# Performance work log

Hardware: AMD Instinct MI355X
Metric: run time of the kernel (lower is better)

Reference implementation:

```python
import jax, jax.numpy as jnp
import numpy as np

EMBED, IN_DIM, HID, LAYERS, NVIEW = 1024, 256, 256, 3, 6


def _lstm_layer(x_seq, Wih, Whh, bih, bhh):
    # x_seq: [BM, N, D]; torch LSTM gate order i,f,g,o
    BM = x_seq.shape[0]
    h0 = jnp.zeros((BM, HID), x_seq.dtype)
    c0 = jnp.zeros((BM, HID), x_seq.dtype)

    def step(carry, x_t):
        h, c = carry
        gates = x_t @ Wih.T + bih + h @ Whh.T + bhh  # [BM, 4H]
        i, f, g, o = jnp.split(gates, 4, axis=-1)
        c = jax.nn.sigmoid(f) * c + jax.nn.sigmoid(i) * jnp.tanh(g)
        h = jax.nn.sigmoid(o) * jnp.tanh(c)
        return (h, c), h

    _, ys = jax.lax.scan(step, (h0, c0), jnp.swapaxes(x_seq, 0, 1))
    return jnp.swapaxes(ys, 0, 1)  # [BM, N, H]


def setup_inputs() -> dict:
    key = jax.random.key(0)
    ks = jax.random.split(key, 16)
    B, M = 32, 256
    s = lambda fan: 1.0 / np.sqrt(fan)
    inp = {
        "b_x_swin": jax.random.normal(ks[0], (B, M, NVIEW, EMBED), jnp.float32),
        "b_x_conv": jax.random.normal(ks[1], (B, M, NVIEW, EMBED), jnp.float32),
        "Wc": jax.random.uniform(ks[2], (EMBED, EMBED), jnp.float32, -s(EMBED), s(EMBED)),
        "bc": jax.random.uniform(ks[3], (EMBED,), jnp.float32, -s(EMBED), s(EMBED)),
        "Win": jax.random.uniform(ks[4], (IN_DIM, EMBED), jnp.float32, -s(EMBED), s(EMBED)),
        "b_in": jax.random.uniform(ks[5], (IN_DIM,), jnp.float32, -s(EMBED), s(EMBED)),
        "Wih": jax.random.uniform(ks[6], (LAYERS, 4 * HID, IN_DIM), jnp.float32, -s(HID), s(HID)),
        "Whh": jax.random.uniform(ks[7], (LAYERS, 4 * HID, HID), jnp.float32, -s(HID), s(HID)),
        "bih": jax.random.uniform(ks[8], (LAYERS, 4 * HID), jnp.float32, -s(HID), s(HID)),
        "bhh": jax.random.uniform(ks[9], (LAYERS, 4 * HID), jnp.float32, -s(HID), s(HID)),
        "Wv": jax.random.uniform(ks[10], (1, HID), jnp.float32, -s(HID), s(HID)),
        "bv": jax.random.uniform(ks[11], (1,), jnp.float32, -s(HID), s(HID)),
        "Ws": jax.random.uniform(ks[12], (1, NVIEW), jnp.float32, -s(NVIEW), s(NVIEW)),
        "bs": jax.random.uniform(ks[13], (1,), jnp.float32, -s(NVIEW), s(NVIEW)),
    }
    return inp


def reference(b_x_swin, b_x_conv, Wc, bc, Win, b_in, Wih, Whh, bih, bhh, Wv, bv, Ws, bs):
    B, M, N, C = b_x_swin.shape
    # fc_conv + exact GELU + residual (vectorized over all samples; same math as per-sample loop)
    x = b_x_swin + jax.nn.gelu(b_x_conv @ Wc.T + bc, approximate=False)
    x = x @ Win.T + b_in                         # [B, M, N, IN_DIM]
    x = x.reshape(B * M, N, IN_DIM)              # LSTM batch = B*M, seq = N
    for l in range(LAYERS):
        x = _lstm_layer(x, Wih[l], Whh[l], bih[l], bhh[l])
    v = (x @ Wv.T + bv).reshape(B, M, N)         # fc_viewport + flatten(1)
    score = (v @ Ws.T + bs).squeeze(-1)          # fc_score -> [B, M]
    return jnp.mean(score, axis=1)               # torch.mean per sample -> [B]
```

## Files before the change

### kernel.cpp

```cpp
#include <hip/hip_runtime.h>
#include <math.h>
#include <stdint.h>

typedef unsigned short u16;
typedef float f32x4 __attribute__((ext_vector_type(4)));
typedef short bf16x8 __attribute__((ext_vector_type(8)));

#define NVIEW 6

__device__ __forceinline__ u16 f2bf(float f){
  unsigned u = __float_as_uint(f);
  u += 0x7FFFu + ((u >> 16) & 1u);
  return (u16)(u >> 16);
}
__device__ __forceinline__ float bf2f(u16 h){
  return __uint_as_float(((unsigned)h) << 16);
}
__device__ __forceinline__ float fsig(float x){
  x = fminf(fmaxf(x, -30.f), 30.f);
  return 1.0f / (1.0f + __expf(-x));
}
__device__ __forceinline__ float ftanh(float x){
  x = fminf(fmaxf(x, -15.f), 15.f);
  float e = __expf(2.0f * x);
  return (e - 1.0f) / (e + 1.0f);
}
__device__ __forceinline__ float gelu_exact(float v){
  float x  = v * 0.70710678118654752f;
  float ax = fabsf(x);
  float t  = 1.0f / fmaf(0.3275911f, ax, 1.0f);
  float p  = t * fmaf(t, fmaf(t, fmaf(t, fmaf(t, 1.061405429f, -1.453152027f),
                                      1.421413741f), -0.284496736f), 0.254829592f);
  float er = copysignf(1.0f - p * __expf(-ax * ax), x);
  return 0.5f * v * (1.0f + er);
}
__device__ __forceinline__ void gload16(const u16* g, u16* l){
  __builtin_amdgcn_global_load_lds((const __attribute__((address_space(1))) unsigned int*)g,
                                   (__attribute__((address_space(3))) unsigned int*)l,
                                   16, 0, 0);
}

__global__ void k_cvt(const float* __restrict__ in, u16* __restrict__ out, long n4){
  long i = (long)blockIdx.x * blockDim.x + threadIdx.x;
  long stride = (long)gridDim.x * blockDim.x;
  for (; i < n4; i += stride){
    const float4 v = ((const float4*)in)[i];
    ushort4 o;
    o.x = f2bf(v.x); o.y = f2bf(v.y); o.z = f2bf(v.z); o.w = f2bf(v.w);
    ((ushort4*)out)[i] = o;
  }
}

__global__ void k_build_wl(const float* __restrict__ Wih, const float* __restrict__ Whh,
                           u16* __restrict__ Wl){
  int idx = blockIdx.x * 256 + threadIdx.x;
  int l   = idx >> 19;
  int rem = idx & 524287;
  int ro  = rem >> 9;
  int k   = rem & 511;
  int u = ro >> 2, q = ro & 3;
  int ri = q * 256 + u;
  float v = (k < 256) ? Wih[(l * 1024 + ri) * 256 + k]
                      : Whh[(l * 1024 + ri) * 256 + (k - 256)];
  Wl[idx] = f2bf(v);
}

__global__ void k_build_bias(const float* __restrict__ bih, const float* __restrict__ bhh,
                             float* __restrict__ biasL, u16* __restrict__ zbuf){
  int idx = blockIdx.x * 256 + threadIdx.x;
  if (idx < 3072){
    int l = idx >> 10; int ro = idx & 1023;
    int u = ro >> 2, q = ro & 3;
    int ri = q * 256 + u;
    biasL[idx] = bih[l * 1024 + ri] + bhh[l * 1024 + ri];
  }
  if (idx < 256) zbuf[idx] = 0;
}

template<int EPI>
__global__ __launch_bounds__(256, 2)
void gemm_dr(const u16* __restrict__ A0, long sA0,
             const u16* __restrict__ A1, long sA1, int K0,
             const u16* __restrict__ Bm, long sB,
             int N, int K,
             const float* __restrict__ bias,
             const float* __restrict__ resid,
             u16* __restrict__ outb,
             float* __restrict__ cbuf,
             int tstep)
{
  __shared__ __align__(16) u16 lA[5 * 4096];
  __shared__ __align__(16) u16 lB[5 * 4096];

  const int tid  = threadIdx.x;
  const int lane = tid & 63;
  const int wid  = tid >> 6;
  const int wm = wid >> 1, wn = wid & 1;
  const int l15 = lane & 15, lk = lane >> 4;
  const long m0 = (long)blockIdx.x * 128;
  const int  n0 = blockIdx.y * 128;
  const int  NT = K >> 5;

  const int rA0  = tid >> 2;
  const int cA   = tid & 3;
  const int scol = (cA ^ (rA0 & 3)) << 3;
  const int ldst = rA0 * 32 + cA * 8;

  auto STAGE = [&](int slot, int t){
    const int kb = t << 5;
    const int so = slot * 4096;
    #pragma unroll
    for (int c = 0; c < 2; ++c){
      const int r  = c * 64 + rA0;
      const int gc = kb + scol;
      const u16* s = (gc < K0) ? (A0 + (m0 + r) * sA0 + gc)
                               : (A1 + (m0 + r) * sA1 + (gc - K0));
      gload16(s, &lA[so + c * 2048 + ldst]);
    }
    #pragma unroll
    for (int c = 0; c < 2; ++c){
      const int r = c * 64 + rA0;
      gload16(Bm + (long)(n0 + r) * sB + (kb + scol), &lB[so + c * 2048 + ldst]);
    }
  };

  f32x4 acc[4][4];
  #pragma unroll
  for (int i = 0; i < 4; ++i)
    #pragma unroll
    for (int j = 0; j < 4; ++j)
      acc[i][j] = (f32x4){0.f, 0.f, 0.f, 0.f};

  const int rdA = (wm * 64 + l15) * 32 + ((lk ^ (l15 & 3)) << 3);
  const int rdB = (wn * 64 + l15) * 32 + ((lk ^ (l15 & 3)) << 3);

  auto COMPUTE = [&](int slot){
    const int so = slot * 4096;
    bf16x8 af[4], bq[4];
    #pragma unroll
    for (int mf = 0; mf < 4; ++mf)
      af[mf] = *(const bf16x8*)&lA[so + rdA + mf * 512];
    #pragma unroll
    for (int nf = 0; nf < 4; ++nf)
      bq[nf] = *(const bf16x8*)&lB[so + rdB + nf * 512];
    #pragma unroll
    for (int mf = 0; mf < 4; ++mf)
      #pragma unroll
      for (int nf = 0; nf < 4; ++nf)
        acc[mf][nf] = __builtin_amdgcn_mfma_f32_16x16x32_bf16(af[mf], bq[nf], acc[mf][nf], 0, 0, 0);
  };

  STAGE(0, 0); STAGE(1, 1); STAGE(2, 2); STAGE(3, 3);

  int sr = 0, sw = 4;
  for (int t = 0; t + 4 <= NT; ++t){
    asm volatile("s_waitcnt vmcnt(12)" ::: "memory");
    asm volatile("s_barrier" ::: "memory");
    if (t + 4 < NT){ STAGE(sw, t + 4); }
    COMPUTE(sr);
    sr = (sr == 4) ? 0 : sr + 1;
    sw = (sw == 4) ? 0 : sw + 1;
  }
  asm volatile("s_waitcnt vmcnt(8)" ::: "memory");
  asm volatile("s_barrier" ::: "memory");
  COMPUTE(sr); sr = (sr == 4) ? 0 : sr + 1;
  asm volatile("s_waitcnt vmcnt(4)" ::: "memory");
  asm volatile("s_barrier" ::: "memory");
  COMPUTE(sr); sr = (sr == 4) ? 0 : sr + 1;
  asm volatile("s_waitcnt vmcnt(0)" ::: "memory");
  asm volatile("s_barrier" ::: "memory");
  COMPUTE(sr);

  if (EPI == 0 || EPI == 1){
    #pragma unroll
    for (int mf = 0; mf < 4; ++mf){
      #pragma unroll
      for (int nf = 0; nf < 4; ++nf){
        int  n    = n0 + wn * 64 + nf * 16 + l15;
        long mrow = m0 + wm * 64 + mf * 16 + lk * 4;
        float bz = bias[n];
        #pragma unroll
        for (int r = 0; r < 4; ++r){
          float v = acc[mf][nf][r] + bz;
          long off = (mrow + r) * N + n;
          if (EPI == 0) v = gelu_exact(v) + resid[off];
          outb[off] = f2bf(v);
        }
      }
    }
  } else {
    const int a  = lane & 3;
    const int qb = lane & ~3;
    #pragma unroll
    for (int mf = 0; mf < 4; ++mf){
      #pragma unroll
      for (int nf = 0; nf < 4; ++nf){
        int n = n0 + wn * 64 + nf * 16 + l15;
        float bz = bias[n];
        float v0 = acc[mf][nf][0] + bz;
        float v1 = acc[mf][nf][1] + bz;
        float v2 = acc[mf][nf][2] + bz;
        float v3 = acc[mf][nf][3] + bz;
        float s0 = (a == 0) ? v0 : (a == 1) ? v1 : (a == 2) ? v2 : v3;
        float s1 = (a == 0) ? v1 : (a == 1) ? v2 : (a == 2) ? v3 : v0;
        float s2 = (a == 0) ? v2 : (a == 1) ? v3 : (a == 2) ? v0 : v1;
        float s3 = (a == 0) ? v3 : (a == 1) ? v0 : (a == 2) ? v1 : v2;
        float r0 = s0;
        float r1 = __shfl(s1, qb + ((a + 3) & 3));
        float r2 = __shfl(s2, qb + ((a + 2) & 3));
        float r3 = __shfl(s3, qb + ((a + 1) & 3));
        float wi = (a == 0) ? r0 : (a == 1) ? r1 : (a == 2) ? r2 : r3;
        float wf = (a == 1) ? r0 : (a == 2) ? r1 : (a == 3) ? r2 : r3;
        float wg = (a == 2) ? r0 : (a == 3) ? r1 : (a == 0) ? r2 : r3;
        float wo = (a == 3) ? r0 : (a == 0) ? r1 : (a == 1) ? r2 : r3;
        long row = m0 + wm * 64 + mf * 16 + lk * 4 + a;
        int  u   = ((n0 + wn * 64 + nf * 16) >> 2) + (l15 >> 2);
        float c_old = (tstep == 0) ? 0.0f : cbuf[row * 256 + u];
        float ii = fsig(wi), ff = fsig(wf), gg = ftanh(wg), oo = fsig(wo);
        float cn = ff * c_old + ii * gg;
        float hn = oo * ftanh(cn);
        cbuf[row * 256 + u] = cn;
        outb[(row * NVIEW + tstep) * 256 + u] = f2bf(hn);
      }
    }
  }
}

__global__ void k_score(const u16* __restrict__ X3, const float* __restrict__ Wv,
                        const float* __restrict__ bv, const float* __restrict__ Ws,
                        const float* __restrict__ bs, float* __restrict__ score){
  int lane = threadIdx.x & 63;
  int bm = blockIdx.x * 4 + (threadIdx.x >> 6);
  const u16* row = X3 + (long)bm * (NVIEW * 256);
  float4 wv = *(const float4*)(Wv + lane * 4);
  float p = 0.f;
  #pragma unroll
  for (int n = 0; n < NVIEW; ++n){
    ushort4 xv = *(const ushort4*)(row + n * 256 + lane * 4);
    float d = bf2f(xv.x) * wv.x + bf2f(xv.y) * wv.y + bf2f(xv.z) * wv.z + bf2f(xv.w) * wv.w;
    p += Ws[n] * d;
  }
  #pragma unroll
  for (int off = 32; off; off >>= 1) p += __shfl_xor(p, off);
  if (lane == 0){
    float sw = Ws[0] + Ws[1] + Ws[2] + Ws[3] + Ws[4] + Ws[5];
    score[bm] = p + bv[0] * sw + bs[0];
  }
}

__global__ void k_mean(const float* __restrict__ score, float* __restrict__ out){
  __shared__ float red[256];
  int b = blockIdx.x, tid = threadIdx.x;
  red[tid] = score[b * 256 + tid];
  __syncthreads();
  for (int s = 128; s > 0; s >>= 1){
    if (tid < s) red[tid] += red[tid + s];
    __syncthreads();
  }
  if (tid == 0) out[b] = red[0] * (1.0f / 256.0f);
}

extern "C" void kernel_launch(void* const* d_in, const int* in_sizes, int n_in,
                              void* d_out, int out_size, void* d_ws, size_t ws_size,
                              hipStream_t stream){
  const float* swin = (const float*)d_in[0];
  const float* conv = (const float*)d_in[1];
  const float* Wc   = (const float*)d_in[2];
  const float* bc   = (const float*)d_in[3];
  const float* Win  = (const float*)d_in[4];
  const float* b_in = (const float*)d_in[5];
  const float* Wih  = (const float*)d_in[6];
  const float* Whh  = (const float*)d_in[7];
  const float* bih  = (const float*)d_in[8];
  const float* bhh  = (const float*)d_in[9];
  const float* Wv   = (const float*)d_in[10];
  const float* bv   = (const float*)d_in[11];
  const float* Ws   = (const float*)d_in[12];
  const float* bs   = (const float*)d_in[13];
  float* out = (float*)d_out;

  char* w = (char*)d_ws;
  u16*  convb = (u16*)(w);
  u16*  X0    = (u16*)(w);
  u16*  XA    = (u16*)(w + 25165824);
  u16*  XB    = (u16*)(w + 50331648);
  float* cbuf = (float*)(w + 75497472);
  u16*  Y     = (u16*)(w + 100663296);
  u16*  Wcb   = (u16*)(w + 201326592);
  u16*  Winb  = (u16*)(w + 203423744);
  u16*  Wl    = (u16*)(w + 203948032);
  float* biasL= (float*)(w + 207093760);
  u16*  zbuf  = (u16*)(w + 207106048);
  float* scoreb = (float*)(w + 207106560);

  k_cvt<<<4096, 256, 0, stream>>>(conv, convb, 49152L * 1024 / 4);
  k_cvt<<<512, 256, 0, stream>>>(Wc, Wcb, 1048576 / 4);
  k_cvt<<<128, 256, 0, stream>>>(Win, Winb, 262144 / 4);
  k_build_wl<<<6144, 256, 0, stream>>>(Wih, Whh, Wl);
  k_build_bias<<<12, 256, 0, stream>>>(bih, bhh, biasL, zbuf);

  gemm_dr<0><<<dim3(384, 8), 256, 0, stream>>>(
      convb, 1024L, convb, 1024L, 1024,
      Wcb, 1024L, 1024, 1024, bc, swin, Y, (float*)nullptr, 0);

  gemm_dr<1><<<dim3(384, 2), 256, 0, stream>>>(
      Y, 1024L, Y, 1024L, 1024,
      Winb, 1024L, 256, 1024, b_in, (const float*)nullptr, X0, (float*)nullptr, 0);

  const u16* xin = X0;
  u16* xout = XA;
  for (int l = 0; l < 3; ++l){
    for (int t = 0; t < 6; ++t){
      const u16* a1 = (t == 0) ? zbuf : (xout + (t - 1) * 256);
      long s1 = (t == 0) ? 0L : 1536L;
      gemm_dr<2><<<dim3(64, 8), 256, 0, stream>>>(
          xin + t * 256, 1536L, a1, s1, 256,
          Wl + l * 1024 * 512, 512L, 1024, 512,
          biasL + l * 1024, (const float*)nullptr,
          xout, cbuf, t);
    }
    if (l == 0){ xin = XA; xout = XB; }
    else if (l == 1){ xin = XB; xout = XA; }
  }

  k_score<<<2048, 256, 0, stream>>>(XA, Wv, bv, Ws, bs, scoreb);
  k_mean<<<32, 256, 0, stream>>>(scoreb, out);
}
```

Measured before the change: 756.1 us.

## Swizzle GEMM workgroup order across XCDs and use wider LDS bank swizzle

Replaces the 2D grid with a 1D grid whose block index is remapped so that consecutive blocks on the same XCD (index mod 8) cover contiguous tiles, aiming to improve L2 reuse of A/B tiles on the multi-die MI355X. It also changes the LDS staging layout to pair rows into 64-element lines with an 8-way XOR swizzle, intended to reduce bank conflicts on the fragment reads. The remapping assumes the grid size is divisible by 8, and the LDS layout change must stay consistent between stores and reads.

```diff
diff --git a/kernel.cpp b/kernel.cpp
--- a/kernel.cpp
+++ b/kernel.cpp
@@ -82,7 +82,7 @@
 void gemm_dr(const u16* __restrict__ A0, long sA0,
              const u16* __restrict__ A1, long sA1, int K0,
              const u16* __restrict__ Bm, long sB,
-             int N, int K,
+             int N, int K, int NBn,
              const float* __restrict__ bias,
              const float* __restrict__ resid,
              u16* __restrict__ outb,
@@ -97,13 +97,20 @@
   const int wid  = tid >> 6;
   const int wm = wid >> 1, wn = wid & 1;
   const int l15 = lane & 15, lk = lane >> 4;
-  const long m0 = (long)blockIdx.x * 128;
-  const int  n0 = blockIdx.y * 128;
+
+  const int nwg = gridDim.x;
+  const int qx  = nwg >> 3;
+  const int bb  = blockIdx.x;
+  const int swz = (bb & 7) * qx + (bb >> 3);
+  const long m0 = (long)(swz / NBn) * 128;
+  const int  n0 = (swz % NBn) * 128;
   const int  NT = K >> 5;
 
-  const int rA0  = tid >> 2;
-  const int cA   = tid & 3;
-  const int scol = (cA ^ (rA0 & 3)) << 3;
+  const int rA0 = tid >> 2;
+  const int cA  = tid & 3;
+  const int slog = (((rA0 & 1) << 2) | cA) ^ ((rA0 >> 1) & 7);
+  const int srow = (rA0 & ~1) | (slog >> 2);
+  const int scol = (slog & 3) << 3;
   const int ldst = rA0 * 32 + cA * 8;
 
   auto STAGE = [&](int slot, int t){
@@ -111,7 +118,7 @@
     const int so = slot * 4096;
     #pragma unroll
     for (int c = 0; c < 2; ++c){
-      const int r  = c * 64 + rA0;
+      const int r  = c * 64 + srow;
       const int gc = kb + scol;
       const u16* s = (gc < K0) ? (A0 + (m0 + r) * sA0 + gc)
                                : (A1 + (m0 + r) * sA1 + (gc - K0));
@@ -119,8 +126,9 @@
     }
     #pragma unroll
     for (int c = 0; c < 2; ++c){
-      const int r = c * 64 + rA0;
-      gload16(Bm + (long)(n0 + r) * sB + (kb + scol), &lB[so + c * 2048 + ldst]);
+      const int r  = c * 64 + srow;
+      const int gc = kb + scol;
+      gload16(Bm + (long)(n0 + r) * sB + gc, &lB[so + c * 2048 + ldst]);
     }
   };
 
@@ -131,8 +139,9 @@
     for (int j = 0; j < 4; ++j)
       acc[i][j] = (f32x4){0.f, 0.f, 0.f, 0.f};
 
-  const int rdA = (wm * 64 + l15) * 32 + ((lk ^ (l15 & 3)) << 3);
-  const int rdB = (wn * 64 + l15) * 32 + ((lk ^ (l15 & 3)) << 3);
+  const int spA = (((l15 & 1) << 2) | lk) ^ (l15 >> 1);
+  const int rdA = (wm * 32 + (l15 >> 1)) * 64 + spA * 8;
+  const int rdB = (wn * 32 + (l15 >> 1)) * 64 + spA * 8;
 
   auto COMPUTE = [&](int slot){
     const int so = slot * 4096;
@@ -299,13 +308,13 @@
   k_build_wl<<<6144, 256, 0, stream>>>(Wih, Whh, Wl);
   k_build_bias<<<12, 256, 0, stream>>>(bih, bhh, biasL, zbuf);
 
-  gemm_dr<0><<<dim3(384, 8), 256, 0, stream>>>(
+  gemm_dr<0><<<3072, 256, 0, stream>>>(
       convb, 1024L, convb, 1024L, 1024,
-      Wcb, 1024L, 1024, 1024, bc, swin, Y, (float*)nullptr, 0);
-
-  gemm_dr<1><<<dim3(384, 2), 256, 0, stream>>>(
+      Wcb, 1024L, 1024, 1024, 8, bc, swin, Y, (float*)nullptr, 0);
+
+  gemm_dr<1><<<768, 256, 0, stream>>>(
       Y, 1024L, Y, 1024L, 1024,
-      Winb, 1024L, 256, 1024, b_in, (const float*)nullptr, X0, (float*)nullptr, 0);
+      Winb, 1024L, 256, 1024, 2, b_in, (const float*)nullptr, X0, (float*)nullptr, 0);
 
   const u16* xin = X0;
   u16* xout = XA;
@@ -313,9 +322,9 @@
     for (int t = 0; t < 6; ++t){
       const u16* a1 = (t == 0) ? zbuf : (xout + (t - 1) * 256);
       long s1 = (t == 0) ? 0L : 1536L;
-      gemm_dr<2><<<dim3(64, 8), 256, 0, stream>>>(
+      gemm_dr<2><<<512, 256, 0, stream>>>(
           xin + t * 256, 1536L, a1, s1, 256,
-          Wl + l * 1024 * 512, 512L, 1024, 512,
+          Wl + l * 1024 * 512, 512L, 1024, 512, 8,
           biasL + l * 1024, (const float*)nullptr,
           xout, cbuf, t);
     }
```

After: 739.1 us. 1.02x faster.
